# Kernel optimization log

Hardware: AMD Instinct MI355X
Metric: run time of the kernel (lower is better)

Reference implementation:

```python
import jax, jax.numpy as jnp
import numpy as np

B, NC, D, C, HM = 4096, 32, 128, 256, 2
H = HM * D
EPS = 1e-5


def _ln(x, g, b):
    mu = jnp.mean(x, axis=-1, keepdims=True)
    var = jnp.mean(jnp.square(x - mu), axis=-1, keepdims=True)
    return (x - mu) * jax.lax.rsqrt(var + EPS) * g + b


def setup_inputs() -> dict:
    key = jax.random.key(0)
    ks = jax.random.split(key, 16)
    s = 0.05
    return {
        "cx": jax.random.normal(ks[0], (B, 16), jnp.float32),
        "cat_vecs": jax.random.normal(ks[1], (B, NC, D), jnp.float32),
        "embed_weights": jax.random.normal(ks[2], (NC, C, D), jnp.float32),
        "Wq": jax.random.normal(ks[3], (NC, D, D), jnp.float32) * s,
        "Wk": jax.random.normal(ks[4], (NC, D, D), jnp.float32) * s,
        "Wv": jax.random.normal(ks[5], (NC, D, D), jnp.float32) * s,
        "ln1_g": jnp.ones((D,), jnp.float32),
        "ln1_b": jnp.zeros((D,), jnp.float32),
        "W1": jax.random.normal(ks[6], (NC, D, H), jnp.float32) * s,
        "b1": jnp.zeros((NC, H), jnp.float32),
        "W2": jax.random.normal(ks[7], (NC, H, D), jnp.float32) * s,
        "b2": jnp.zeros((NC, D), jnp.float32),
        "ln2_g": jnp.ones((D,), jnp.float32),
        "ln2_b": jnp.zeros((D,), jnp.float32),
        "Ws": jax.random.normal(ks[8], (NC, D), jnp.float32) * s,
        "bs": jnp.zeros((NC,), jnp.float32),
    }


def reference(cx, cat_vecs, embed_weights, Wq, Wk, Wv, ln1_g, ln1_b, W1, b1, W2, b2, ln2_g, ln2_b, Ws, bs):
    # cx is unused by the original forward body.
    # Per-feature projections, batched over the Nc axis (j).
    q = jnp.einsum('bjd,jde->bje', cat_vecs, Wq)          # [B, Nc, D]
    k = jnp.einsum('jcd,jde->jce', embed_weights, Wk)     # [Nc, C, D]
    v = jnp.einsum('jcd,jde->jce', embed_weights, Wv)     # [Nc, C, D]
    scores = jnp.einsum('bjd,jcd->bjc', q, k) / jnp.sqrt(jnp.asarray(D, q.dtype))
    alpha = jax.nn.softmax(scores, axis=-1)               # [B, Nc, C]
    h = jnp.einsum('bjc,jcd->bjd', alpha, v)              # [B, Nc, D]
    h = _ln(cat_vecs + h, ln1_g, ln1_b)
    ff = jnp.einsum('bjd,jdh->bjh', h, W1) + b1
    ff = jnp.einsum('bjh,jhd->bjd', jax.nn.relu(ff), W2) + b2
    h = _ln(h + ff, ln2_g, ln2_b)
    out = jax.nn.sigmoid(jnp.einsum('bjd,jd->bj', h, Ws) + bs)  # [B, Nc]
    return out
```

## Files before the change

kernel.cpp:

```cpp
#include <hip/hip_runtime.h>


typedef __attribute__((ext_vector_type(4))) float f32x4;
typedef __attribute__((ext_vector_type(8))) short bf16x8;
typedef __attribute__((ext_vector_type(4))) unsigned u32x4;

#define DEVI static __device__ __forceinline__
#define SB __builtin_amdgcn_sched_barrier(0)
#define BARR __builtin_amdgcn_s_barrier()
#define MEMF asm volatile("" ::: "memory")

constexpr int NC = 32, D = 128, C = 256, H = 256;

DEVI unsigned short f2b(float f) {
  unsigned u = __builtin_bit_cast(unsigned, f);
  u += 0x7fffu + ((u >> 16) & 1u);
  return (unsigned short)(u >> 16);
}
DEVI float b2f(unsigned short h) {
  unsigned u = ((unsigned)h) << 16;
  return __builtin_bit_cast(float, u);
}
DEVI unsigned pk2(float a, float b) {
  return (unsigned)f2b(a) | ((unsigned)f2b(b) << 16);
}
DEVI unsigned cvtpk(float a, float b) {
  unsigned r;
  asm("v_cvt_pk_bf16_f32 %0, %1, %2" : "=v"(r) : "v"(a), "v"(b));
  return r;
}

template <int N> DEVI void vmwait() {
  asm volatile("s_waitcnt vmcnt(%0)" ::"n"(N) : "memory");
}
DEVI void lgkm0() { asm volatile("s_waitcnt lgkmcnt(0)" ::: "memory"); }

DEVI void gload16(const void* g, void* l) {
  __builtin_amdgcn_global_load_lds(
      (const __attribute__((address_space(1))) void*)g,
      (__attribute__((address_space(3))) void*)l, 16, 0, 0);
}


__global__ __launch_bounds__(256) void prepG_kernel(
    const float* __restrict__ Wk, const float* __restrict__ Wq,
    float* __restrict__ G) {
  __shared__ float wqT[128][132];
  __shared__ float wkb[32][132];
  const int j = blockIdx.x >> 2, ft = blockIdx.x & 3;
  const int tid = threadIdx.x;
  for (int i = tid; i < 128 * 32; i += 256) {
    int d = i >> 5, e4 = i & 31;
    float4 v = *(const float4*)(Wq + ((long)j * 128 + d) * 128 + e4 * 4);
    wqT[e4 * 4 + 0][d] = v.x; wqT[e4 * 4 + 1][d] = v.y;
    wqT[e4 * 4 + 2][d] = v.z; wqT[e4 * 4 + 3][d] = v.w;
  }
  for (int i = tid; i < 32 * 32; i += 256) {
    int r = i >> 5, e0 = (i & 31) * 4;
    float4 v = *(const float4*)(Wk + ((long)j * 128 + ft * 32 + r) * 128 + e0);
    wkb[r][e0] = v.x; wkb[r][e0 + 1] = v.y;
    wkb[r][e0 + 2] = v.z; wkb[r][e0 + 3] = v.w;
  }
  __syncthreads();
  const int fl = tid >> 3, s = tid & 7;
  float acc[16];
#pragma unroll
  for (int u = 0; u < 16; ++u) acc[u] = 0.f;
  for (int e = 0; e < 128; ++e) {
    float kk = wkb[fl][e];
#pragma unroll
    for (int u4 = 0; u4 < 4; ++u4) {
      float4 a = *(const float4*)&wqT[e][s * 16 + u4 * 4];
      acc[u4 * 4 + 0] = fmaf(a.x, kk, acc[u4 * 4 + 0]);
      acc[u4 * 4 + 1] = fmaf(a.y, kk, acc[u4 * 4 + 1]);
      acc[u4 * 4 + 2] = fmaf(a.z, kk, acc[u4 * 4 + 2]);
      acc[u4 * 4 + 3] = fmaf(a.w, kk, acc[u4 * 4 + 3]);
    }
  }
  float* gout = G + (long)j * 16384 + (ft * 32 + fl) * 128 + s * 16;
#pragma unroll
  for (int u4 = 0; u4 < 4; ++u4) {
    float4 v = {acc[u4 * 4 + 0], acc[u4 * 4 + 1], acc[u4 * 4 + 2], acc[u4 * 4 + 3]};
    *(float4*)(gout + u4 * 4) = v;
  }
}

__global__ __launch_bounds__(256) void prepA_kernel(
    const float* __restrict__ emb, const float* __restrict__ G,
    const float* __restrict__ Wv, const float* __restrict__ W1,
    const float* __restrict__ W2, unsigned short* __restrict__ MtP,
    unsigned short* __restrict__ VtP, unsigned short* __restrict__ W1tP,
    unsigned short* __restrict__ W2tP) {
  __shared__ __align__(16) char smemraw[49152];
  const int bid = blockIdx.x, tid = threadIdx.x;
  if (bid < 512) {
    const bool isV = bid >= 256;
    const int bb = isV ? bid - 256 : bid;
    const int j = bb >> 3, ct = bb & 7;
    unsigned short* wmh = (unsigned short*)smemraw;
    float* eb = (float*)(smemraw + 32768);
    const float4* gw = (const float4*)((isV ? Wv : G) + (long)j * D * D);
    for (int i = tid; i < D * D / 4; i += 256) {
      float4 v = gw[i];
      uint2 pk = {cvtpk(v.x, v.y), cvtpk(v.z, v.w)};
      ((uint2*)wmh)[i] = pk;
    }
    const float4* ge = (const float4*)(emb + ((long)j * C + ct * 32) * D);
    float4* le = (float4*)eb;
    for (int i = tid; i < 32 * D / 4; i += 256) le[i] = ge[i];
    __syncthreads();
    const int eq = (tid & 31) * 4;
    const int cg = (tid >> 5) * 4;
    float acc[4][4];
#pragma unroll
    for (int ci = 0; ci < 4; ++ci)
#pragma unroll
      for (int ei = 0; ei < 4; ++ei) acc[ci][ei] = 0.f;
    for (int d = 0; d < 128; ++d) {
      uint2 wv = *(const uint2*)((const char*)wmh + d * 256 + eq * 2);
      float w0 = b2f((unsigned short)(wv.x & 0xffff));
      float w1 = b2f((unsigned short)(wv.x >> 16));
      float w2 = b2f((unsigned short)(wv.y & 0xffff));
      float w3 = b2f((unsigned short)(wv.y >> 16));
#pragma unroll
      for (int ci = 0; ci < 4; ++ci) {
        float ec = eb[(cg + ci) * 128 + d];
        acc[ci][0] = fmaf(ec, w0, acc[ci][0]);
        acc[ci][1] = fmaf(ec, w1, acc[ci][1]);
        acc[ci][2] = fmaf(ec, w2, acc[ci][2]);
        acc[ci][3] = fmaf(ec, w3, acc[ci][3]);
      }
    }
    if (!isV) {
      const float scale = 0.08838834764831845f;
#pragma unroll
      for (int ci = 0; ci < 4; ++ci) {
        int c = ct * 32 + cg + ci;
        long byte = (long)j * 65536 + c * 256 + (((eq >> 3) ^ (c & 7)) << 4) + (eq & 7) * 2;
        uint2 pk = {pk2(acc[ci][0] * scale, acc[ci][1] * scale),
                    pk2(acc[ci][2] * scale, acc[ci][3] * scale)};
        *(uint2*)((char*)MtP + byte) = pk;
      }
    } else {
      const int c0 = ct * 32 + cg;
#pragma unroll
      for (int ei = 0; ei < 4; ++ei) {
        int e = eq + ei;
        long byte = (long)j * 65536 + e * 512 + (((c0 >> 3) ^ (e & 7)) << 4) + (c0 & 7) * 2;
        uint2 pk = {pk2(acc[0][ei], acc[1][ei]),
                    pk2(acc[2][ei], acc[3][ei])};
        *(uint2*)((char*)VtP + byte) = pk;
      }
    }
  } else {
    float(*t)[33] = reinterpret_cast<float(*)[33]>(smemraw);
    const int idx = bid - 512;
    const bool isW2 = idx >= 1024;
    const int bb = isW2 ? idx - 1024 : idx;
    const int j = bb >> 5, tile = bb & 31;
    const int rr = tid >> 3, c4 = tid & 7;
    if (!isW2) {
      const int dt = tile & 3, ht = tile >> 2;
      float4 v = *(const float4*)(W1 + ((long)j * 128 + dt * 32 + rr) * 256 + ht * 32 + c4 * 4);
      t[rr][c4 * 4 + 0] = v.x; t[rr][c4 * 4 + 1] = v.y;
      t[rr][c4 * 4 + 2] = v.z; t[rr][c4 * 4 + 3] = v.w;
      __syncthreads();
      int row = ht * 32 + rr, colb = dt * 32 + c4 * 4;
      uint2 pk = {pk2(t[c4 * 4 + 0][rr], t[c4 * 4 + 1][rr]),
                  pk2(t[c4 * 4 + 2][rr], t[c4 * 4 + 3][rr])};
      long byte = (long)j * 65536 + row * 256 + (((colb >> 3) ^ (row & 7)) << 4) + (colb & 7) * 2;
      *(uint2*)((char*)W1tP + byte) = pk;
    } else {
      const int et = tile & 3, ht = tile >> 2;
      float4 v = *(const float4*)(W2 + ((long)j * 256 + ht * 32 + rr) * 128 + et * 32 + c4 * 4);
      t[rr][c4 * 4 + 0] = v.x; t[rr][c4 * 4 + 1] = v.y;
      t[rr][c4 * 4 + 2] = v.z; t[rr][c4 * 4 + 3] = v.w;
      __syncthreads();
      int row = et * 32 + rr, colb = ht * 32 + c4 * 4;
      uint2 pk = {pk2(t[c4 * 4 + 0][rr], t[c4 * 4 + 1][rr]),
                  pk2(t[c4 * 4 + 2][rr], t[c4 * 4 + 3][rr])};
      long byte = (long)j * 65536 + row * 512 + (((colb >> 3) ^ (row & 7)) << 4) + (colb & 7) * 2;
      *(uint2*)((char*)W2tP + byte) = pk;
    }
  }
}

__global__ __launch_bounds__(256, 4) void fused_kernel(
    const float* __restrict__ x, const unsigned short* __restrict__ MtP,
    const unsigned short* __restrict__ VtP, const unsigned short* __restrict__ W1tP,
    const unsigned short* __restrict__ W2tP, const float* __restrict__ b1,
    const float* __restrict__ b2, const float* __restrict__ g1,
    const float* __restrict__ be1, const float* __restrict__ g2,
    const float* __restrict__ be2, const float* __restrict__ Ws,
    const float* __restrict__ bs, float* __restrict__ out) {
  __shared__ __align__(16) unsigned short wb[2][8192];
  __shared__ __align__(16) float sv[1024];
  const int bid = blockIdx.x;
  const int wg = (bid & 7) * 256 + (bid >> 3);
  const int j = wg >> 6, b0 = (wg & 63) * 64;
  const int tid = threadIdx.x, w = tid >> 6, l = tid & 63, lr = l & 15, lg = l >> 4;
  const int bloc = w * 16 + lr;

  const unsigned short* pnl0 = MtP + (long)j * 32768;
  const unsigned short* pnl1 = VtP + (long)j * 32768;
  const unsigned short* pnl2 = W1tP + (long)j * 32768;
  const unsigned short* pnl3 = W2tP + (long)j * 32768;

  auto ISSUE = [&](int s2) {
    const unsigned short* base = (s2 < 4) ? pnl0 : (s2 < 8) ? pnl1 : (s2 < 12) ? pnl2 : pnl3;
    const char* gq = (const char*)(base + (s2 & 3) * 8192);
    char* lb = (char*)&wb[s2 & 1][0] + w * 4096;
    SB;
#pragma unroll
    for (int t = 0; t < 4; ++t)
      gload16(gq + (w * 4 + t) * 1024 + l * 16, lb + t * 1024);
    SB;
  };

  const float* xrow = x + ((long)(b0 + bloc) * NC + j) * D;
  float4 xf[4][2];
#pragma unroll
  for (int kc = 0; kc < 4; ++kc) {
    xf[kc][0] = *(const float4*)(xrow + kc * 32 + lg * 8);
    xf[kc][1] = *(const float4*)(xrow + kc * 32 + lg * 8 + 4);
  }
  for (int i = tid; i < 1024; i += 256) {
    float v;
    if (i < 256) v = b1[j * H + i];
    else if (i < 384) v = b2[j * D + i - 256];
    else if (i < 512) v = g1[i - 384];
    else if (i < 640) v = be1[i - 512];
    else if (i < 768) v = g2[i - 640];
    else if (i < 896) v = be2[i - 768];
    else v = Ws[j * D + i - 896];
    sv[i] = v;
  }
  SB;
  ISSUE(0);
  ISSUE(1);
  float bsj = bs[j];
  bf16x8 xa[4];
#pragma unroll
  for (int kc = 0; kc < 4; ++kc) {
    u32x4 t;
    t[0] = cvtpk(xf[kc][0].x, xf[kc][0].y);
    t[1] = cvtpk(xf[kc][0].z, xf[kc][0].w);
    t[2] = cvtpk(xf[kc][1].x, xf[kc][1].y);
    t[3] = cvtpk(xf[kc][1].z, xf[kc][1].w);
    xa[kc] = __builtin_bit_cast(bf16x8, t);
  }
  lgkm0(); SB; BARR; MEMF; SB;

  int inner[4], inner2[8];
#pragma unroll
  for (int kc = 0; kc < 4; ++kc)
    inner[kc] = lr * 256 + (((kc * 4 + lg) ^ (lr & 7)) << 4);
#pragma unroll
  for (int kc = 0; kc < 8; ++kc)
    inner2[kc] = lr * 512 + (((kc * 4 + lg) ^ (lr & 7)) << 4);

  const int ad0 = (((lg & 1) << 5) + lr) << 2;
  const int ad1 = ad0 + 64;
  const bool hi = (lg >> 1) != 0;

  bf16x8 aa[8], xa2[4], aa2[8];
  unsigned hb[8][2];
  float4 xr[8];

  f32x4 sc[16];
#pragma unroll
  for (int t = 0; t < 16; ++t) sc[t] = (f32x4){0.f, 0.f, 0.f, 0.f};
#pragma unroll
  for (int q = 0; q < 4; ++q) {
    vmwait<4>(); SB; BARR; MEMF; SB;
    const char* wp = (const char*)wb[q & 1];
    __builtin_amdgcn_s_setprio(1);
#pragma unroll
    for (int c4 = 0; c4 < 4; ++c4)
#pragma unroll
      for (int kc = 0; kc < 4; ++kc) {
        bf16x8 bf = *(const bf16x8*)(wp + c4 * 4096 + inner[kc]);
        sc[q * 4 + c4] =
            __builtin_amdgcn_mfma_f32_16x16x32_bf16(bf, xa[kc], sc[q * 4 + c4], 0, 0, 0);
      }
    __builtin_amdgcn_s_setprio(0);
    if (q == 3) {
      float mx = -1e30f;
#pragma unroll
      for (int ct = 0; ct < 16; ++ct)
#pragma unroll
        for (int i = 0; i < 4; ++i) mx = fmaxf(mx, sc[ct][i]);
      mx = fmaxf(mx, __shfl_xor(mx, 16));
      mx = fmaxf(mx, __shfl_xor(mx, 32));
      float sm = 0.f;
#pragma unroll
      for (int ct = 0; ct < 16; ++ct)
#pragma unroll
        for (int i = 0; i < 4; ++i) {
          float e = __expf(sc[ct][i] - mx);
          sc[ct][i] = e;
          sm += e;
        }
      sm += __shfl_xor(sm, 16);
      sm += __shfl_xor(sm, 32);
      float inv = 1.f / sm;
      unsigned au[16][2];
#pragma unroll
      for (int ct = 0; ct < 16; ++ct) {
        au[ct][0] = cvtpk(sc[ct][0] * inv, sc[ct][1] * inv);
        au[ct][1] = cvtpk(sc[ct][2] * inv, sc[ct][3] * inv);
      }
#pragma unroll
      for (int kc = 0; kc < 8; ++kc) {
        u32x4 t;
#pragma unroll
        for (int h = 0; h < 2; ++h) {
          int ad = h ? ad1 : ad0;
#pragma unroll
          for (int p = 0; p < 2; ++p) {
            int f0 = __builtin_amdgcn_ds_bpermute(ad, (int)au[2 * kc][p]);
            int f1 = __builtin_amdgcn_ds_bpermute(ad, (int)au[2 * kc + 1][p]);
            t[h * 2 + p] = (unsigned)(hi ? f1 : f0);
          }
        }
        aa[kc] = __builtin_bit_cast(bf16x8, t);
      }
    }
    lgkm0(); SB; BARR; MEMF; SB;
    ISSUE(q + 2);
  }

  f32x4 ha[8];
#pragma unroll
  for (int t = 0; t < 8; ++t) ha[t] = (f32x4){0.f, 0.f, 0.f, 0.f};
#pragma unroll
  for (int q = 0; q < 4; ++q) {
    vmwait<4>(); SB; BARR; MEMF; SB;
    const char* wp = (const char*)wb[q & 1];
    __builtin_amdgcn_s_setprio(1);
#pragma unroll
    for (int e2 = 0; e2 < 2; ++e2)
#pragma unroll
      for (int kc = 0; kc < 8; ++kc) {
        bf16x8 bf = *(const bf16x8*)(wp + e2 * 8192 + inner2[kc]);
        ha[q * 2 + e2] =
            __builtin_amdgcn_mfma_f32_16x16x32_bf16(bf, aa[kc], ha[q * 2 + e2], 0, 0, 0);
      }
    __builtin_amdgcn_s_setprio(0);
    if (q == 2) {
#pragma unroll
      for (int et = 0; et < 8; ++et)
        xr[et] = *(const float4*)(xrow + et * 16 + lg * 4);
    }
    if (q == 3) {
      float hvv[8][4];
      float s1 = 0.f, s2s = 0.f;
#pragma unroll
      for (int et = 0; et < 8; ++et)
#pragma unroll
        for (int i = 0; i < 4; ++i) {
          float v = ha[et][i] + xr[et][i];
          hvv[et][i] = v;
          s1 += v;
          s2s += v * v;
        }
      s1 += __shfl_xor(s1, 16); s2s += __shfl_xor(s2s, 16);
      s1 += __shfl_xor(s1, 32); s2s += __shfl_xor(s2s, 32);
      float mu = s1 * (1.f / 128.f);
      float var = s2s * (1.f / 128.f) - mu * mu;
      float rs = rsqrtf(var + 1e-5f);
#pragma unroll
      for (int et = 0; et < 8; ++et) {
        f32x4 gg = *(const f32x4*)&sv[384 + et * 16 + lg * 4];
        f32x4 bb = *(const f32x4*)&sv[512 + et * 16 + lg * 4];
        float h0 = (hvv[et][0] - mu) * rs * gg[0] + bb[0];
        float h1n = (hvv[et][1] - mu) * rs * gg[1] + bb[1];
        float h2 = (hvv[et][2] - mu) * rs * gg[2] + bb[2];
        float h3 = (hvv[et][3] - mu) * rs * gg[3] + bb[3];
        hb[et][0] = cvtpk(h0, h1n);
        hb[et][1] = cvtpk(h2, h3);
      }
#pragma unroll
      for (int kc = 0; kc < 4; ++kc) {
        u32x4 t;
#pragma unroll
        for (int h = 0; h < 2; ++h) {
          int ad = h ? ad1 : ad0;
#pragma unroll
          for (int p = 0; p < 2; ++p) {
            int f0 = __builtin_amdgcn_ds_bpermute(ad, (int)hb[2 * kc][p]);
            int f1 = __builtin_amdgcn_ds_bpermute(ad, (int)hb[2 * kc + 1][p]);
            t[h * 2 + p] = (unsigned)(hi ? f1 : f0);
          }
        }
        xa2[kc] = __builtin_bit_cast(bf16x8, t);
      }
    }
    lgkm0(); SB; BARR; MEMF; SB;
    ISSUE(6 + q);
  }

  unsigned ffu[16][2];
#pragma unroll
  for (int q = 0; q < 4; ++q) {
    vmwait<4>(); SB; BARR; MEMF; SB;
    const char* wp = (const char*)wb[q & 1];
    f32x4 fa4[4];
#pragma unroll
    for (int t = 0; t < 4; ++t) fa4[t] = (f32x4){0.f, 0.f, 0.f, 0.f};
    __builtin_amdgcn_s_setprio(1);
#pragma unroll
    for (int c4 = 0; c4 < 4; ++c4)
#pragma unroll
      for (int kc = 0; kc < 4; ++kc) {
        bf16x8 bf = *(const bf16x8*)(wp + c4 * 4096 + inner[kc]);
        fa4[c4] =
            __builtin_amdgcn_mfma_f32_16x16x32_bf16(bf, xa2[kc], fa4[c4], 0, 0, 0);
      }
    __builtin_amdgcn_s_setprio(0);
#pragma unroll
    for (int c4 = 0; c4 < 4; ++c4) {
      int ht = q * 4 + c4;
      f32x4 bb = *(const f32x4*)&sv[ht * 16 + lg * 4];
      float v0 = fmaxf(fa4[c4][0] + bb[0], 0.f);
      float v1 = fmaxf(fa4[c4][1] + bb[1], 0.f);
      float v2 = fmaxf(fa4[c4][2] + bb[2], 0.f);
      float v3 = fmaxf(fa4[c4][3] + bb[3], 0.f);
      ffu[ht][0] = cvtpk(v0, v1);
      ffu[ht][1] = cvtpk(v2, v3);
    }
    if (q == 3) {
#pragma unroll
      for (int kc = 0; kc < 8; ++kc) {
        u32x4 t;
#pragma unroll
        for (int h = 0; h < 2; ++h) {
          int ad = h ? ad1 : ad0;
#pragma unroll
          for (int p = 0; p < 2; ++p) {
            int f0 = __builtin_amdgcn_ds_bpermute(ad, (int)ffu[2 * kc][p]);
            int f1 = __builtin_amdgcn_ds_bpermute(ad, (int)ffu[2 * kc + 1][p]);
            t[h * 2 + p] = (unsigned)(hi ? f1 : f0);
          }
        }
        aa2[kc] = __builtin_bit_cast(bf16x8, t);
      }
    }
    lgkm0(); SB; BARR; MEMF; SB;
    ISSUE(10 + q);
  }

  f32x4 oa[8];
#pragma unroll
  for (int t = 0; t < 8; ++t) oa[t] = (f32x4){0.f, 0.f, 0.f, 0.f};
#pragma unroll
  for (int q = 0; q < 4; ++q) {
    if (q == 3) { vmwait<0>(); } else { vmwait<4>(); }
    SB; BARR; MEMF; SB;
    const char* wp = (const char*)wb[q & 1];
    __builtin_amdgcn_s_setprio(1);
#pragma unroll
    for (int e2 = 0; e2 < 2; ++e2)
#pragma unroll
      for (int kc = 0; kc < 8; ++kc) {
        bf16x8 bf = *(const bf16x8*)(wp + e2 * 8192 + inner2[kc]);
        oa[q * 2 + e2] =
            __builtin_amdgcn_mfma_f32_16x16x32_bf16(bf, aa2[kc], oa[q * 2 + e2], 0, 0, 0);
      }
    __builtin_amdgcn_s_setprio(0);
    if (q < 3) {
      lgkm0(); SB; BARR; MEMF; SB;
      if (q < 2) ISSUE(14 + q);
    }
  }
  {
    float t1 = 0.f, t2 = 0.f;
#pragma unroll
    for (int et = 0; et < 8; ++et) {
      f32x4 bb = *(const f32x4*)&sv[256 + et * 16 + lg * 4];
      float r0 = b2f((unsigned short)(hb[et][0] & 0xffff));
      float r1 = b2f((unsigned short)(hb[et][0] >> 16));
      float r2 = b2f((unsigned short)(hb[et][1] & 0xffff));
      float r3 = b2f((unsigned short)(hb[et][1] >> 16));
      float v0 = oa[et][0] + bb[0] + r0;
      float v1 = oa[et][1] + bb[1] + r1;
      float v2 = oa[et][2] + bb[2] + r2;
      float v3 = oa[et][3] + bb[3] + r3;
      oa[et][0] = v0; oa[et][1] = v1; oa[et][2] = v2; oa[et][3] = v3;
      t1 += (v0 + v1) + (v2 + v3);
      t2 += (v0 * v0 + v1 * v1) + (v2 * v2 + v3 * v3);
    }
    t1 += __shfl_xor(t1, 16); t2 += __shfl_xor(t2, 16);
    t1 += __shfl_xor(t1, 32); t2 += __shfl_xor(t2, 32);
    float mu2 = t1 * (1.f / 128.f);
    float var = t2 * (1.f / 128.f) - mu2 * mu2;
    float rs2 = rsqrtf(var + 1e-5f);
    float lp = 0.f;
#pragma unroll
    for (int et = 0; et < 8; ++et) {
      f32x4 gg = *(const f32x4*)&sv[640 + et * 16 + lg * 4];
      f32x4 bb = *(const f32x4*)&sv[768 + et * 16 + lg * 4];
      f32x4 ww = *(const f32x4*)&sv[896 + et * 16 + lg * 4];
#pragma unroll
      for (int i = 0; i < 4; ++i) {
        float h2 = (oa[et][i] - mu2) * rs2 * gg[i] + bb[i];
        lp = fmaf(h2, ww[i], lp);
      }
    }
    lp += __shfl_xor(lp, 16);
    lp += __shfl_xor(lp, 32);
    if (lg == 0) {
      float sg = 1.f / (1.f + __expf(-(lp + bsj)));
      out[(long)(b0 + bloc) * NC + j] = sg;
    }
  }
}

extern "C" void kernel_launch(void* const* d_in, const int* in_sizes, int n_in,
                              void* d_out, int out_size, void* d_ws,
                              size_t ws_size, hipStream_t stream) {
  (void)in_sizes; (void)n_in; (void)out_size; (void)ws_size;
  const float* cat = (const float*)d_in[1];
  const float* emb = (const float*)d_in[2];
  const float* Wq = (const float*)d_in[3];
  const float* Wk = (const float*)d_in[4];
  const float* Wv = (const float*)d_in[5];
  const float* g1 = (const float*)d_in[6];
  const float* be1 = (const float*)d_in[7];
  const float* W1 = (const float*)d_in[8];
  const float* b1 = (const float*)d_in[9];
  const float* W2 = (const float*)d_in[10];
  const float* b2 = (const float*)d_in[11];
  const float* g2 = (const float*)d_in[12];
  const float* be2 = (const float*)d_in[13];
  const float* Ws = (const float*)d_in[14];
  const float* bs = (const float*)d_in[15];
  float* out = (float*)d_out;

  char* ws = (char*)d_ws;
  unsigned short* MtP = (unsigned short*)(ws);
  unsigned short* VtP = (unsigned short*)(ws + (2 << 20));
  unsigned short* W1tP = (unsigned short*)(ws + (4 << 20));
  unsigned short* W2tP = (unsigned short*)(ws + (6 << 20));
  float* G = (float*)(ws + (8 << 20));

  prepG_kernel<<<128, 256, 0, stream>>>(Wk, Wq, G);
  prepA_kernel<<<2560, 256, 0, stream>>>(emb, G, Wv, W1, W2, MtP, VtP, W1tP, W2tP);
  fused_kernel<<<2048, 256, 0, stream>>>(cat, MtP, VtP, W1tP, W2tP, b1, b2, g1,
                                         be1, g2, be2, Ws, bs, out);
}
```

Before: 110.6 us.

## Fold Wq·Wk precompute into prep kernel and batch weight transpose tiles

Removes the separate prepG launch that built G = Wq·Wkᵀ per feature. Each M-block now first computes K = emb·Wk in bf16 and then multiplies by a transposed bf16 Wq in shared memory. This reassociates the product and drops one kernel launch plus the G round trip through global memory. W1/W2 transpose blocks now each handle four tiles, cutting the grid from 2560 to 1024 blocks, while the extra bf16 rounding of K and Wq may change accuracy slightly.

```diff
diff --git a/kernel.cpp b/kernel.cpp
--- a/kernel.cpp
+++ b/kernel.cpp
@@ -42,64 +42,108 @@
 }
 
 
-__global__ __launch_bounds__(256) void prepG_kernel(
-    const float* __restrict__ Wk, const float* __restrict__ Wq,
-    float* __restrict__ G) {
-  __shared__ float wqT[128][132];
-  __shared__ float wkb[32][132];
-  const int j = blockIdx.x >> 2, ft = blockIdx.x & 3;
-  const int tid = threadIdx.x;
-  for (int i = tid; i < 128 * 32; i += 256) {
-    int d = i >> 5, e4 = i & 31;
-    float4 v = *(const float4*)(Wq + ((long)j * 128 + d) * 128 + e4 * 4);
-    wqT[e4 * 4 + 0][d] = v.x; wqT[e4 * 4 + 1][d] = v.y;
-    wqT[e4 * 4 + 2][d] = v.z; wqT[e4 * 4 + 3][d] = v.w;
-  }
-  for (int i = tid; i < 32 * 32; i += 256) {
-    int r = i >> 5, e0 = (i & 31) * 4;
-    float4 v = *(const float4*)(Wk + ((long)j * 128 + ft * 32 + r) * 128 + e0);
-    wkb[r][e0] = v.x; wkb[r][e0 + 1] = v.y;
-    wkb[r][e0 + 2] = v.z; wkb[r][e0 + 3] = v.w;
-  }
-  __syncthreads();
-  const int fl = tid >> 3, s = tid & 7;
-  float acc[16];
-#pragma unroll
-  for (int u = 0; u < 16; ++u) acc[u] = 0.f;
-  for (int e = 0; e < 128; ++e) {
-    float kk = wkb[fl][e];
-#pragma unroll
-    for (int u4 = 0; u4 < 4; ++u4) {
-      float4 a = *(const float4*)&wqT[e][s * 16 + u4 * 4];
-      acc[u4 * 4 + 0] = fmaf(a.x, kk, acc[u4 * 4 + 0]);
-      acc[u4 * 4 + 1] = fmaf(a.y, kk, acc[u4 * 4 + 1]);
-      acc[u4 * 4 + 2] = fmaf(a.z, kk, acc[u4 * 4 + 2]);
-      acc[u4 * 4 + 3] = fmaf(a.w, kk, acc[u4 * 4 + 3]);
-    }
-  }
-  float* gout = G + (long)j * 16384 + (ft * 32 + fl) * 128 + s * 16;
-#pragma unroll
-  for (int u4 = 0; u4 < 4; ++u4) {
-    float4 v = {acc[u4 * 4 + 0], acc[u4 * 4 + 1], acc[u4 * 4 + 2], acc[u4 * 4 + 3]};
-    *(float4*)(gout + u4 * 4) = v;
-  }
-}
-
 __global__ __launch_bounds__(256) void prepA_kernel(
-    const float* __restrict__ emb, const float* __restrict__ G,
-    const float* __restrict__ Wv, const float* __restrict__ W1,
-    const float* __restrict__ W2, unsigned short* __restrict__ MtP,
-    unsigned short* __restrict__ VtP, unsigned short* __restrict__ W1tP,
-    unsigned short* __restrict__ W2tP) {
+    const float* __restrict__ emb, const float* __restrict__ Wk,
+    const float* __restrict__ Wq, const float* __restrict__ Wv,
+    const float* __restrict__ W1, const float* __restrict__ W2,
+    unsigned short* __restrict__ MtP, unsigned short* __restrict__ VtP,
+    unsigned short* __restrict__ W1tP, unsigned short* __restrict__ W2tP) {
   __shared__ __align__(16) char smemraw[49152];
   const int bid = blockIdx.x, tid = threadIdx.x;
-  if (bid < 512) {
-    const bool isV = bid >= 256;
-    const int bb = isV ? bid - 256 : bid;
+  if (bid < 256) {
+    const int j = bid >> 3, ct = bid & 7;
+    unsigned short* A = (unsigned short*)smemraw;
+    unsigned short* ebB = (unsigned short*)(smemraw + 32768);
+    unsigned short* Kb = (unsigned short*)(smemraw + 40960);
+    const float4* gk = (const float4*)(Wk + (long)j * D * D);
+    for (int i = tid; i < D * D / 4; i += 256) {
+      float4 v = gk[i];
+      uint2 pk = {cvtpk(v.x, v.y), cvtpk(v.z, v.w)};
+      ((uint2*)A)[i] = pk;
+    }
+    const float4* ge = (const float4*)(emb + ((long)j * C + ct * 32) * D);
+    for (int i = tid; i < 32 * D / 4; i += 256) {
+      float4 v = ge[i];
+      uint2 pk = {cvtpk(v.x, v.y), cvtpk(v.z, v.w)};
+      ((uint2*)ebB)[i] = pk;
+    }
+    __syncthreads();
+    const int eq = (tid & 31) * 4;
+    const int cg = (tid >> 5) * 4;
+    {
+      float acc[4][4];
+#pragma unroll
+      for (int ci = 0; ci < 4; ++ci)
+#pragma unroll
+        for (int ei = 0; ei < 4; ++ei) acc[ci][ei] = 0.f;
+      for (int d = 0; d < 128; ++d) {
+        uint2 wv = *(const uint2*)((const char*)A + d * 256 + eq * 2);
+        float w0 = b2f((unsigned short)(wv.x & 0xffff));
+        float w1 = b2f((unsigned short)(wv.x >> 16));
+        float w2 = b2f((unsigned short)(wv.y & 0xffff));
+        float w3 = b2f((unsigned short)(wv.y >> 16));
+#pragma unroll
+        for (int ci = 0; ci < 4; ++ci) {
+          float ec = b2f(*(const unsigned short*)((const char*)ebB + (cg + ci) * 256 + d * 2));
+          acc[ci][0] = fmaf(ec, w0, acc[ci][0]);
+          acc[ci][1] = fmaf(ec, w1, acc[ci][1]);
+          acc[ci][2] = fmaf(ec, w2, acc[ci][2]);
+          acc[ci][3] = fmaf(ec, w3, acc[ci][3]);
+        }
+      }
+#pragma unroll
+      for (int ci = 0; ci < 4; ++ci) {
+        uint2 pk = {cvtpk(acc[ci][0], acc[ci][1]), cvtpk(acc[ci][2], acc[ci][3])};
+        *(uint2*)((char*)Kb + (cg + ci) * 256 + eq * 2) = pk;
+      }
+    }
+    __syncthreads();
+    for (int i = tid; i < D * D / 4; i += 256) {
+      int d = i >> 5, e4 = (i & 31) * 4;
+      float4 v = *(const float4*)(Wq + ((long)j * 128 + d) * 128 + e4);
+      *(unsigned short*)((char*)A + (e4 + 0) * 256 + d * 2) = f2b(v.x);
+      *(unsigned short*)((char*)A + (e4 + 1) * 256 + d * 2) = f2b(v.y);
+      *(unsigned short*)((char*)A + (e4 + 2) * 256 + d * 2) = f2b(v.z);
+      *(unsigned short*)((char*)A + (e4 + 3) * 256 + d * 2) = f2b(v.w);
+    }
+    __syncthreads();
+    {
+      float acc[4][4];
+#pragma unroll
+      for (int ci = 0; ci < 4; ++ci)
+#pragma unroll
+        for (int di = 0; di < 4; ++di) acc[ci][di] = 0.f;
+      for (int e = 0; e < 128; ++e) {
+        uint2 wv = *(const uint2*)((const char*)A + e * 256 + eq * 2);
+        float w0 = b2f((unsigned short)(wv.x & 0xffff));
+        float w1 = b2f((unsigned short)(wv.x >> 16));
+        float w2 = b2f((unsigned short)(wv.y & 0xffff));
+        float w3 = b2f((unsigned short)(wv.y >> 16));
+#pragma unroll
+        for (int ci = 0; ci < 4; ++ci) {
+          float kk = b2f(*(const unsigned short*)((const char*)Kb + (cg + ci) * 256 + e * 2));
+          acc[ci][0] = fmaf(kk, w0, acc[ci][0]);
+          acc[ci][1] = fmaf(kk, w1, acc[ci][1]);
+          acc[ci][2] = fmaf(kk, w2, acc[ci][2]);
+          acc[ci][3] = fmaf(kk, w3, acc[ci][3]);
+        }
+      }
+      const float scale = 0.08838834764831845f;
+#pragma unroll
+      for (int ci = 0; ci < 4; ++ci) {
+        int c = ct * 32 + cg + ci;
+        long byte = (long)j * 65536 + c * 256 + (((eq >> 3) ^ (c & 7)) << 4) + (eq & 7) * 2;
+        uint2 pk = {pk2(acc[ci][0] * scale, acc[ci][1] * scale),
+                    pk2(acc[ci][2] * scale, acc[ci][3] * scale)};
+        *(uint2*)((char*)MtP + byte) = pk;
+      }
+    }
+  } else if (bid < 512) {
+    const int bb = bid - 256;
     const int j = bb >> 3, ct = bb & 7;
     unsigned short* wmh = (unsigned short*)smemraw;
     float* eb = (float*)(smemraw + 32768);
-    const float4* gw = (const float4*)((isV ? Wv : G) + (long)j * D * D);
+    const float4* gw = (const float4*)(Wv + (long)j * D * D);
     for (int i = tid; i < D * D / 4; i += 256) {
       float4 v = gw[i];
       uint2 pk = {cvtpk(v.x, v.y), cvtpk(v.z, v.w)};
@@ -131,56 +175,58 @@
         acc[ci][3] = fmaf(ec, w3, acc[ci][3]);
       }
     }
-    if (!isV) {
-      const float scale = 0.08838834764831845f;
-#pragma unroll
-      for (int ci = 0; ci < 4; ++ci) {
-        int c = ct * 32 + cg + ci;
-        long byte = (long)j * 65536 + c * 256 + (((eq >> 3) ^ (c & 7)) << 4) + (eq & 7) * 2;
-        uint2 pk = {pk2(acc[ci][0] * scale, acc[ci][1] * scale),
-                    pk2(acc[ci][2] * scale, acc[ci][3] * scale)};
-        *(uint2*)((char*)MtP + byte) = pk;
-      }
-    } else {
-      const int c0 = ct * 32 + cg;
-#pragma unroll
-      for (int ei = 0; ei < 4; ++ei) {
-        int e = eq + ei;
-        long byte = (long)j * 65536 + e * 512 + (((c0 >> 3) ^ (e & 7)) << 4) + (c0 & 7) * 2;
-        uint2 pk = {pk2(acc[0][ei], acc[1][ei]),
-                    pk2(acc[2][ei], acc[3][ei])};
-        *(uint2*)((char*)VtP + byte) = pk;
-      }
+    const int c0 = ct * 32 + cg;
+#pragma unroll
+    for (int ei = 0; ei < 4; ++ei) {
+      int e = eq + ei;
+      long byte = (long)j * 65536 + e * 512 + (((c0 >> 3) ^ (e & 7)) << 4) + (c0 & 7) * 2;
+      uint2 pk = {pk2(acc[0][ei], acc[1][ei]),
+                  pk2(acc[2][ei], acc[3][ei])};
+      *(uint2*)((char*)VtP + byte) = pk;
     }
   } else {
-    float(*t)[33] = reinterpret_cast<float(*)[33]>(smemraw);
+    float(*t)[32][33] = reinterpret_cast<float(*)[32][33]>(smemraw);
     const int idx = bid - 512;
-    const bool isW2 = idx >= 1024;
-    const int bb = isW2 ? idx - 1024 : idx;
-    const int j = bb >> 5, tile = bb & 31;
+    const bool isW2 = idx >= 256;
+    const int bb = idx & 255;
+    const int j = bb >> 3, tq = bb & 7;
     const int rr = tid >> 3, c4 = tid & 7;
     if (!isW2) {
-      const int dt = tile & 3, ht = tile >> 2;
-      float4 v = *(const float4*)(W1 + ((long)j * 128 + dt * 32 + rr) * 256 + ht * 32 + c4 * 4);
-      t[rr][c4 * 4 + 0] = v.x; t[rr][c4 * 4 + 1] = v.y;
-      t[rr][c4 * 4 + 2] = v.z; t[rr][c4 * 4 + 3] = v.w;
+#pragma unroll
+      for (int k = 0; k < 4; ++k) {
+        int tile = tq * 4 + k, dt = tile & 3, ht = tile >> 2;
+        float4 v = *(const float4*)(W1 + ((long)j * 128 + dt * 32 + rr) * 256 + ht * 32 + c4 * 4);
+        t[k][rr][c4 * 4 + 0] = v.x; t[k][rr][c4 * 4 + 1] = v.y;
+        t[k][rr][c4 * 4 + 2] = v.z; t[k][rr][c4 * 4 + 3] = v.w;
+      }
       __syncthreads();
-      int row = ht * 32 + rr, colb = dt * 32 + c4 * 4;
-      uint2 pk = {pk2(t[c4 * 4 + 0][rr], t[c4 * 4 + 1][rr]),
-                  pk2(t[c4 * 4 + 2][rr], t[c4 * 4 + 3][rr])};
-      long byte = (long)j * 65536 + row * 256 + (((colb >> 3) ^ (row & 7)) << 4) + (colb & 7) * 2;
-      *(uint2*)((char*)W1tP + byte) = pk;
+#pragma unroll
+      for (int k = 0; k < 4; ++k) {
+        int tile = tq * 4 + k, dt = tile & 3, ht = tile >> 2;
+        int row = ht * 32 + rr, colb = dt * 32 + c4 * 4;
+        uint2 pk = {pk2(t[k][c4 * 4 + 0][rr], t[k][c4 * 4 + 1][rr]),
+                    pk2(t[k][c4 * 4 + 2][rr], t[k][c4 * 4 + 3][rr])};
+        long byte = (long)j * 65536 + row * 256 + (((colb >> 3) ^ (row & 7)) << 4) + (colb & 7) * 2;
+        *(uint2*)((char*)W1tP + byte) = pk;
+      }
     } else {
-      const int et = tile & 3, ht = tile >> 2;
-      float4 v = *(const float4*)(W2 + ((long)j * 256 + ht * 32 + rr) * 128 + et * 32 + c4 * 4);
-      t[rr][c4 * 4 + 0] = v.x; t[rr][c4 * 4 + 1] = v.y;
-      t[rr][c4 * 4 + 2] = v.z; t[rr][c4 * 4 + 3] = v.w;
+#pragma unroll
+      for (int k = 0; k < 4; ++k) {
+        int tile = tq * 4 + k, et = tile & 3, ht = tile >> 2;
+        float4 v = *(const float4*)(W2 + ((long)j * 256 + ht * 32 + rr) * 128 + et * 32 + c4 * 4);
+        t[k][rr][c4 * 4 + 0] = v.x; t[k][rr][c4 * 4 + 1] = v.y;
+        t[k][rr][c4 * 4 + 2] = v.z; t[k][rr][c4 * 4 + 3] = v.w;
+      }
       __syncthreads();
-      int row = et * 32 + rr, colb = ht * 32 + c4 * 4;
-      uint2 pk = {pk2(t[c4 * 4 + 0][rr], t[c4 * 4 + 1][rr]),
-                  pk2(t[c4 * 4 + 2][rr], t[c4 * 4 + 3][rr])};
-      long byte = (long)j * 65536 + row * 512 + (((colb >> 3) ^ (row & 7)) << 4) + (colb & 7) * 2;
-      *(uint2*)((char*)W2tP + byte) = pk;
+#pragma unroll
+      for (int k = 0; k < 4; ++k) {
+        int tile = tq * 4 + k, et = tile & 3, ht = tile >> 2;
+        int row = et * 32 + rr, colb = ht * 32 + c4 * 4;
+        uint2 pk = {pk2(t[k][c4 * 4 + 0][rr], t[k][c4 * 4 + 1][rr]),
+                    pk2(t[k][c4 * 4 + 2][rr], t[k][c4 * 4 + 3][rr])};
+        long byte = (long)j * 65536 + row * 512 + (((colb >> 3) ^ (row & 7)) << 4) + (colb & 7) * 2;
+        *(uint2*)((char*)W2tP + byte) = pk;
+      }
     }
   }
 }
@@ -542,10 +588,9 @@
   unsigned short* VtP = (unsigned short*)(ws + (2 << 20));
   unsigned short* W1tP = (unsigned short*)(ws + (4 << 20));
   unsigned short* W2tP = (unsigned short*)(ws + (6 << 20));
-  float* G = (float*)(ws + (8 << 20));
-
-  prepG_kernel<<<128, 256, 0, stream>>>(Wk, Wq, G);
-  prepA_kernel<<<2560, 256, 0, stream>>>(emb, G, Wv, W1, W2, MtP, VtP, W1tP, W2tP);
+
+  prepA_kernel<<<1024, 256, 0, stream>>>(emb, Wk, Wq, Wv, W1, W2, MtP, VtP,
+                                         W1tP, W2tP);
   fused_kernel<<<2048, 256, 0, stream>>>(cat, MtP, VtP, W1tP, W2tP, b1, b2, g1,
                                          be1, g2, be2, Ws, bs, out);
 }
```

New measurement: 106.6 us. 3.6% less time.
